# Optimization experiments

Measured on AMD Instinct MI355X. Metric: run time of the kernel, lower is better.

Reference implementation:

```python
import jax, jax.numpy as jnp
import numpy as np

HIDDEN = 2048
INTER = 1024
N_EXPERTS = 8
TOP_K = 2
B, S = 1, 2048


def setup_inputs() -> dict:
    key = jax.random.key(0)
    k1, k2, k3, k4, k5, k6 = jax.random.split(key, 6)
    x = jax.random.normal(k1, (B, S, HIDDEN), dtype=jnp.float32)
    expert_indices = jax.random.randint(k2, (B, S, TOP_K), 0, N_EXPERTS, dtype=jnp.int64)
    expert_weights = jax.random.uniform(k3, (B, S, TOP_K), dtype=jnp.float32)
    gate_proj = jax.random.normal(k4, (N_EXPERTS, INTER, HIDDEN), dtype=jnp.float32) * 0.02
    up_proj = jax.random.normal(k5, (N_EXPERTS, INTER, HIDDEN), dtype=jnp.float32) * 0.02
    down_proj = jax.random.normal(k6, (N_EXPERTS, HIDDEN, INTER), dtype=jnp.float32) * 0.02
    return {"x": x, "expert_indices": expert_indices, "expert_weights": expert_weights,
            "gate_proj": gate_proj, "up_proj": up_proj, "down_proj": down_proj}


def reference(x, expert_indices, expert_weights, gate_proj, up_proj, down_proj):
    b, s, h = x.shape
    e = gate_proj.shape[0]
    xf = x.reshape(-1, h)                                   # [T, H]
    idx = expert_indices.reshape(-1, expert_indices.shape[-1])   # [T, K]
    wts = expert_weights.reshape(-1, expert_weights.shape[-1])   # [T, K]
    # Combine weights per (token, expert); duplicate expert slots sum, matching index_add_.
    comb = jnp.sum(jax.nn.one_hot(idx, e, dtype=xf.dtype) * wts[..., None], axis=1)  # [T, E]
    # SwiGLU expert MLP, computed densely over all experts then masked by routing weights.
    g = jnp.einsum('th,eih->tei', xf, gate_proj)            # [T, E, I]
    u = jnp.einsum('th,eih->tei', xf, up_proj)              # [T, E, I]
    inter = jax.nn.silu(g) * u                              # [T, E, I]
    out = jnp.einsum('tei,ehi->th', inter * comb[:, :, None], down_proj)  # [T, H]
    return out.reshape(b, s, h)
```

## Files before the change

### kernel.cpp

```cpp
#include <hip/hip_runtime.h>
#include <math.h>

#define HID 2048
#define ITR 1024
#define NEXP 8
#define TOPK 2
#define NTOK 2048
#define NSLOT (NTOK * TOPK)
#define MAXTT 40
#define SLOTS 80

typedef __attribute__((ext_vector_type(8))) short short8;
typedef __attribute__((ext_vector_type(4))) float f32x4;

__device__ __forceinline__ unsigned short f2bf(float f) {
    unsigned u = __float_as_uint(f);
    u += 0x7FFFu + ((u >> 16) & 1u);
    return (unsigned short)(u >> 16);
}

#define GLL16(g, l) \
    __builtin_amdgcn_global_load_lds((const __attribute__((address_space(1))) unsigned int*)(g), \
                                     (__attribute__((address_space(3))) unsigned int*)(l), 16, 0, 0)

__global__ void route_all_k(const int* __restrict__ idx,
                            const float* __restrict__ wts,
                            int* __restrict__ counts_g,
                            int* __restrict__ btok,
                            float* __restrict__ bw,
                            int* __restrict__ offs_g,
                            int* __restrict__ slotmap,
                            int* __restrict__ gu_tab,
                            int* __restrict__ dn_tab) {
    __shared__ int h[NEXP], nt[NEXP], pre[NEXP], base[NEXP], cur[NEXP];
    const int tid = threadIdx.x;
    if (tid < NEXP) { h[tid] = 0; cur[tid] = 0; }
    __syncthreads();
    for (int s = tid; s < NSLOT; s += 256) atomicAdd(&h[idx[s]], 1);
    __syncthreads();
    if (tid == 0) {
        int a = 0;
        for (int e = 0; e < NEXP; ++e) {
            base[e] = a; counts_g[e] = h[e]; offs_g[e] = a;
            int t = (h[e] + 127) >> 7; nt[e] = t; a += t << 7;
        }
        int p = 0;
        for (int e = 0; e < NEXP; ++e) { pre[e] = p; p += nt[e]; }
    }
    __syncthreads();
    for (int s = tid; s < NSLOT; s += 256) {
        int e = idx[s];
        int p = atomicAdd(&cur[e], 1);
        btok[e * NSLOT + p] = s >> 1;
        bw[e * NSLOT + p] = wts[s];
        slotmap[s] = base[e] + p;
    }
    for (int i = tid; i < 8 * SLOTS; i += 256) { gu_tab[i] = -1; dn_tab[i] = -1; }
    __syncthreads();
    if (tid < 128) {
        int c = tid, e = c >> 4, ib = c & 15;
        int sb = 2 * pre[e] + (ib >> 3) * nt[e];
        for (int j = 0; j < nt[e]; ++j)
            gu_tab[(sb + j) * 8 + (ib & 7)] = (e << 16) | (ib << 8) | j;
    } else {
        int c = tid - 128, e = c >> 4, ib = c & 15;
        int sb = 2 * pre[e] + (ib >> 3) * nt[e];
        for (int j = 0; j < nt[e]; ++j)
            dn_tab[(sb + j) * 8 + (ib & 7)] = (e << 16) | (ib << 8) | j;
    }
}

__device__ __forceinline__ void cvt8(const float* __restrict__ src,
                                     unsigned short* __restrict__ dst, size_t o) {
    const float4* s4 = (const float4*)src + o * 2;
    float4 a = s4[0], b = s4[1];
    union { unsigned short s[8]; uint4 v; } r;
    r.s[0] = f2bf(a.x); r.s[1] = f2bf(a.y); r.s[2] = f2bf(a.z); r.s[3] = f2bf(a.w);
    r.s[4] = f2bf(b.x); r.s[5] = f2bf(b.y); r.s[6] = f2bf(b.z); r.s[7] = f2bf(b.w);
    ((uint4*)dst)[o] = r.v;
}

__global__ void cvt_gux_k(const float* __restrict__ x, const float* __restrict__ g,
                          const float* __restrict__ u,
                          unsigned short* __restrict__ xb, unsigned short* __restrict__ gb,
                          unsigned short* __restrict__ ub) {
    size_t j = (size_t)blockIdx.x * 256 + threadIdx.x;
    const size_t X8 = (size_t)NTOK * HID / 8;
    const size_t W8 = (size_t)NEXP * ITR * HID / 8;
    if (j < X8)           cvt8(x, xb, j);
    else if (j < X8 + W8) cvt8(g, gb, j - X8);
    else                  cvt8(u, ub, j - X8 - W8);
}

__global__ void cvt_dn_k(const float* __restrict__ d, unsigned short* __restrict__ db) {
    size_t j = (size_t)blockIdx.x * 256 + threadIdx.x;
    cvt8(d, db, j);
}

__global__ void combine_k(const float* __restrict__ part,
                          const int* __restrict__ slotmap,
                          float* __restrict__ out) {
    int gid = blockIdx.x * 256 + threadIdx.x;
    int t = gid >> 9;
    int c = gid & 511;
    int s0 = slotmap[t * 2], s1 = slotmap[t * 2 + 1];
    float4 a = ((const float4*)part)[(size_t)s0 * 512 + c];
    float4 b = ((const float4*)part)[(size_t)s1 * 512 + c];
    float4 r; r.x = a.x + b.x; r.y = a.y + b.y; r.z = a.z + b.z; r.w = a.w + b.w;
    ((float4*)out)[gid] = r;
}

#define BK 64

__launch_bounds__(256)
__global__ void moe_gu_bf_k(const unsigned short* __restrict__ xb,
                            const unsigned short* __restrict__ gateb,
                            const unsigned short* __restrict__ upb,
                            const int* __restrict__ counts,
                            const int* __restrict__ btok,
                            const int* __restrict__ off,
                            const int* __restrict__ gu_tab,
                            unsigned short* __restrict__ interw) {
    const int v = gu_tab[blockIdx.x];
    if (v < 0) return;
    const int e    = v >> 16;
    const int iblk = (v >> 8) & 255;
    const int tile = v & 255;
    const int n = counts[e];

    __shared__ unsigned short s_a[128 * 64];
    __shared__ unsigned short s_bg[64 * 64];
    __shared__ unsigned short s_bu[64 * 64];
    __shared__ int s_tok[128];

    const int tid = threadIdx.x;
    if (tid < 128) {
        int tt = tile * 128 + tid;
        s_tok[tid] = btok[e * NSLOT + (tt < n ? tt : n - 1)];
    }
    __syncthreads();

    const int w = tid >> 6;
    const int lane = tid & 63;

    const char* asrc[4]; unsigned short* adst[4];
    #pragma unroll
    for (int t = 0; t < 4; ++t) {
        int c = tid + t * 256;
        int r = c >> 3;
        unsigned sw = ((unsigned)(c & 7) * 16u) ^ (((unsigned)r & 7u) << 4);
        asrc[t] = (const char*)xb + (size_t)s_tok[r] * (HID * 2) + sw;
        adst[t] = s_a + (size_t)(t * 256 + w * 64) * 8;
    }
    const char* gB = (const char*)gateb + ((size_t)e * ITR + (size_t)iblk * 64) * (HID * 2);
    const char* uB = (const char*)upb   + ((size_t)e * ITR + (size_t)iblk * 64) * (HID * 2);
    const char* gsrc[2]; const char* usrc[2];
    unsigned short* gdst[2]; unsigned short* udst[2];
    #pragma unroll
    for (int t = 0; t < 2; ++t) {
        int c = tid + t * 256;
        int r = c >> 3;
        unsigned sw = ((unsigned)(c & 7) * 16u) ^ (((unsigned)r & 7u) << 4);
        gsrc[t] = gB + (size_t)r * (HID * 2) + sw;
        usrc[t] = uB + (size_t)r * (HID * 2) + sw;
        gdst[t] = s_bg + (size_t)(t * 256 + w * 64) * 8;
        udst[t] = s_bu + (size_t)(t * 256 + w * 64) * 8;
    }

    const int wm = (w & 1) * 64, wn = (w >> 1) * 32;
    const int l15 = lane & 15, quad = lane >> 4;

    f32x4 accg[4][2], accu[4][2];
    #pragma unroll
    for (int m = 0; m < 4; ++m)
        #pragma unroll
        for (int nn = 0; nn < 2; ++nn) {
            accg[m][nn] = (f32x4){0.f, 0.f, 0.f, 0.f};
            accu[m][nn] = (f32x4){0.f, 0.f, 0.f, 0.f};
        }

    for (int k0 = 0; k0 < HID; k0 += BK) {
        const int kb0 = k0 * 2;
        #pragma unroll
        for (int t = 0; t < 4; ++t) GLL16(asrc[t] + kb0, adst[t]);
        #pragma unroll
        for (int t = 0; t < 2; ++t) { GLL16(gsrc[t] + kb0, gdst[t]); GLL16(usrc[t] + kb0, udst[t]); }
        __syncthreads();
        #pragma unroll
        for (int kk = 0; kk < 2; ++kk) {
            const unsigned kbyte = (unsigned)(kk * 64 + quad * 16);
            short8 af[4], bg[2], bu[2];
            #pragma unroll
            for (int m = 0; m < 4; ++m) {
                unsigned r = (unsigned)(wm + m * 16 + l15);
                af[m] = *(const short8*)&s_a[r * 64 + ((kbyte ^ ((r & 7u) << 4)) >> 1)];
            }
            #pragma unroll
            for (int nn = 0; nn < 2; ++nn) {
                unsigned r = (unsigned)(wn + nn * 16 + l15);
                unsigned co = (kbyte ^ ((r & 7u) << 4)) >> 1;
                bg[nn] = *(const short8*)&s_bg[r * 64 + co];
                bu[nn] = *(const short8*)&s_bu[r * 64 + co];
            }
            #pragma unroll
            for (int m = 0; m < 4; ++m)
                #pragma unroll
                for (int nn = 0; nn < 2; ++nn) {
                    accg[m][nn] = __builtin_amdgcn_mfma_f32_16x16x32_bf16(af[m], bg[nn], accg[m][nn], 0, 0, 0);
                    accu[m][nn] = __builtin_amdgcn_mfma_f32_16x16x32_bf16(af[m], bu[nn], accu[m][nn], 0, 0, 0);
                }
        }
        __syncthreads();
    }

    const int pos0 = off[e] + tile * 128;
    #pragma unroll
    for (int m = 0; m < 4; ++m) {
        #pragma unroll
        for (int nn = 0; nn < 2; ++nn) {
            int col = iblk * 64 + wn + nn * 16 + l15;
            #pragma unroll
            for (int r = 0; r < 4; ++r) {
                int row = wm + m * 16 + quad * 4 + r;
                float g = accg[m][nn][r], u = accu[m][nn][r];
                float s = g / (1.0f + __expf(-g));
                interw[(size_t)(pos0 + row) * ITR + col] = f2bf(s * u);
            }
        }
    }
}

__launch_bounds__(256)
__global__ void moe_down_bf_k(const unsigned short* __restrict__ interw,
                              const unsigned short* __restrict__ downb,
                              const int* __restrict__ counts,
                              const int* __restrict__ btok,
                              const float* __restrict__ bw,
                              const int* __restrict__ off,
                              const int* __restrict__ dn_tab,
                              float* __restrict__ dst,
                              int mode) {
    const int v = dn_tab[blockIdx.x];
    if (v < 0) return;
    const int e    = v >> 16;
    const int hblk = (v >> 8) & 255;
    const int tile = v & 255;
    const int n = counts[e];

    __shared__ unsigned short s_a[128 * 64];
    __shared__ unsigned short s_b[128 * 64];
    __shared__ int s_tok[128];
    __shared__ float s_w[128];

    const int tid = threadIdx.x;
    if (tid < 128) {
        int tt = tile * 128 + tid;
        bool vv = tt < n;
        s_tok[tid] = btok[e * NSLOT + (vv ? tt : n - 1)];
        s_w[tid] = vv ? bw[e * NSLOT + tt] : 0.0f;
    }
    __syncthreads();

    const int w = tid >> 6;
    const int lane = tid & 63;
    const int pos0 = off[e] + tile * 128;

    const char* asrc[4]; unsigned short* adst[4];
    const char* bsrc[4]; unsigned short* bdst[4];
    const char* dB = (const char*)downb + ((size_t)e * HID + (size_t)hblk * 128) * (ITR * 2);
    #pragma unroll
    for (int t = 0; t < 4; ++t) {
        int c = tid + t * 256;
        int r = c >> 3;
        unsigned sw = ((unsigned)(c & 7) * 16u) ^ (((unsigned)r & 7u) << 4);
        asrc[t] = (const char*)interw + (size_t)(pos0 + r) * (ITR * 2) + sw;
        bsrc[t] = dB + (size_t)r * (ITR * 2) + sw;
        adst[t] = s_a + (size_t)(t * 256 + w * 64) * 8;
        bdst[t] = s_b + (size_t)(t * 256 + w * 64) * 8;
    }

    const int wm = (w & 1) * 64, wn = (w >> 1) * 64;
    const int l15 = lane & 15, quad = lane >> 4;

    f32x4 acc[4][4];
    #pragma unroll
    for (int m = 0; m < 4; ++m)
        #pragma unroll
        for (int nn = 0; nn < 4; ++nn) acc[m][nn] = (f32x4){0.f, 0.f, 0.f, 0.f};

    for (int k0 = 0; k0 < ITR; k0 += BK) {
        const int kb0 = k0 * 2;
        #pragma unroll
        for (int t = 0; t < 4; ++t) GLL16(asrc[t] + kb0, adst[t]);
        #pragma unroll
        for (int t = 0; t < 4; ++t) GLL16(bsrc[t] + kb0, bdst[t]);
        __syncthreads();
        #pragma unroll
        for (int kk = 0; kk < 2; ++kk) {
            const unsigned kbyte = (unsigned)(kk * 64 + quad * 16);
            short8 af[4], bf[4];
            #pragma unroll
            for (int m = 0; m < 4; ++m) {
                unsigned r = (unsigned)(wm + m * 16 + l15);
                af[m] = *(const short8*)&s_a[r * 64 + ((kbyte ^ ((r & 7u) << 4)) >> 1)];
            }
            #pragma unroll
            for (int nn = 0; nn < 4; ++nn) {
                unsigned r = (unsigned)(wn + nn * 16 + l15);
                bf[nn] = *(const short8*)&s_b[r * 64 + ((kbyte ^ ((r & 7u) << 4)) >> 1)];
            }
            #pragma unroll
            for (int m = 0; m < 4; ++m)
                #pragma unroll
                for (int nn = 0; nn < 4; ++nn)
                    acc[m][nn] = __builtin_amdgcn_mfma_f32_16x16x32_bf16(af[m], bf[nn], acc[m][nn], 0, 0, 0);
        }
        __syncthreads();
    }

    if (mode == 0) {
        #pragma unroll
        for (int m = 0; m < 4; ++m) {
            #pragma unroll
            for (int nn = 0; nn < 4; ++nn) {
                int col = hblk * 128 + wn + nn * 16 + l15;
                #pragma unroll
                for (int r = 0; r < 4; ++r) {
                    int row = wm + m * 16 + quad * 4 + r;
                    dst[(size_t)(pos0 + row) * HID + col] = s_w[row] * acc[m][nn][r];
                }
            }
        }
    } else {
        #pragma unroll
        for (int m = 0; m < 4; ++m) {
            #pragma unroll
            for (int nn = 0; nn < 4; ++nn) {
                int col = hblk * 128 + wn + nn * 16 + l15;
                #pragma unroll
                for (int r = 0; r < 4; ++r) {
                    int row = wm + m * 16 + quad * 4 + r;
                    atomicAdd(&dst[(size_t)s_tok[row] * HID + col], s_w[row] * acc[m][nn][r]);
                }
            }
        }
    }
}

#define LDW 72

__global__ void xconv_k(const float* __restrict__ x, unsigned short* __restrict__ xb) {
    int i = blockIdx.x * blockDim.x + threadIdx.x;
    float4 v = ((const float4*)x)[i];
    ushort4 b;
    b.x = f2bf(v.x); b.y = f2bf(v.y); b.z = f2bf(v.z); b.w = f2bf(v.w);
    ((ushort4*)xb)[i] = b;
}

__launch_bounds__(256)
__global__ void moe_gu_k(const unsigned short* __restrict__ xb,
                         const float* __restrict__ gate,
                         const float* __restrict__ up,
                         const int* __restrict__ counts,
                         const int* __restrict__ btok,
                         const int* __restrict__ off,
                         const int* __restrict__ gu_tab,
                         unsigned short* __restrict__ interw) {
    const int v = gu_tab[blockIdx.x];
    if (v < 0) return;
    const int e    = v >> 16;
    const int iblk = (v >> 8) & 255;
    const int tile = v & 255;
    const int n = counts[e];

    __shared__ unsigned short s_a[128][LDW];
    __shared__ unsigned short s_bg[64][LDW];
    __shared__ unsigned short s_bu[64][LDW];
    __shared__ int s_tok[128];

    const int tid = threadIdx.x;
    if (tid < 128) {
        int tt = tile * 128 + tid;
        s_tok[tid] = btok[e * NSLOT + (tt < n ? tt : n - 1)];
    }
    __syncthreads();

    const unsigned short* asrc[4];
    unsigned aoff[4];
    #pragma unroll
    for (int t = 0; t < 4; ++t) {
        int c = tid + t * 256;
        int r = c >> 3, col = (c & 7) * 8;
        asrc[t] = xb + (size_t)s_tok[r] * HID + col;
        aoff[t] = r * LDW + col;
    }
    const float* gbase = gate + (size_t)e * ITR * HID + (size_t)iblk * 64 * HID;
    const float* ubase = up   + (size_t)e * ITR * HID + (size_t)iblk * 64 * HID;
    unsigned boff[4], loff[4];
    #pragma unroll
    for (int t = 0; t < 4; ++t) {
        int f = tid + t * 256;
        int r = f >> 4, col = (f & 15) * 4;
        boff[t] = r * HID + col;
        loff[t] = r * LDW + col;
    }

    const int lane = tid & 63;
    const int w = tid >> 6;
    const int wm = (w & 1) * 64, wn = (w >> 1) * 32;
    const int l15 = lane & 15, quad = lane >> 4;

    f32x4 accg[4][2], accu[4][2];
    #pragma unroll
    for (int m = 0; m < 4; ++m)
        #pragma unroll
        for (int nn = 0; nn < 2; ++nn) {
            accg[m][nn] = (f32x4){0.f, 0.f, 0.f, 0.f};
            accu[m][nn] = (f32x4){0.f, 0.f, 0.f, 0.f};
        }

    unsigned short* s_flat_a = &s_a[0][0];
    unsigned short* s_flat_g = &s_bg[0][0];
    unsigned short* s_flat_u = &s_bu[0][0];

    uint4 pa[4];
    float4 pg[4], pu[4];
    #pragma unroll
    for (int t = 0; t < 4; ++t) {
        pa[t] = *(const uint4*)(asrc[t]);
        pg[t] = *(const float4*)(gbase + boff[t]);
        pu[t] = *(const float4*)(ubase + boff[t]);
    }

    for (int k0 = 0; k0 < HID; k0 += BK) {
        #pragma unroll
        for (int t = 0; t < 4; ++t) {
            *(uint4*)(s_flat_a + aoff[t]) = pa[t];
            ushort4 gb, ub;
            gb.x = f2bf(pg[t].x); gb.y = f2bf(pg[t].y); gb.z = f2bf(pg[t].z); gb.w = f2bf(pg[t].w);
            ub.x = f2bf(pu[t].x); ub.y = f2bf(pu[t].y); ub.z = f2bf(pu[t].z); ub.w = f2bf(pu[t].w);
            *(ushort4*)(s_flat_g + loff[t]) = gb;
            *(ushort4*)(s_flat_u + loff[t]) = ub;
        }
        __syncthreads();
        if (k0 + BK < HID) {
            #pragma unroll
            for (int t = 0; t < 4; ++t) {
                pa[t] = *(const uint4*)(asrc[t] + k0 + BK);
                pg[t] = *(const float4*)(gbase + boff[t] + k0 + BK);
                pu[t] = *(const float4*)(ubase + boff[t] + k0 + BK);
            }
        }
        #pragma unroll
        for (int kk = 0; kk < 2; ++kk) {
            const int kc = kk * 32 + quad * 8;
            short8 af[4], bg[2], bu[2];
            #pragma unroll
            for (int m = 0; m < 4; ++m)
                af[m] = *(const short8*)&s_a[wm + m * 16 + l15][kc];
            #pragma unroll
            for (int nn = 0; nn < 2; ++nn) {
                bg[nn] = *(const short8*)&s_bg[wn + nn * 16 + l15][kc];
                bu[nn] = *(const short8*)&s_bu[wn + nn * 16 + l15][kc];
            }
            #pragma unroll
            for (int m = 0; m < 4; ++m)
                #pragma unroll
                for (int nn = 0; nn < 2; ++nn) {
                    accg[m][nn] = __builtin_amdgcn_mfma_f32_16x16x32_bf16(af[m], bg[nn], accg[m][nn], 0, 0, 0);
                    accu[m][nn] = __builtin_amdgcn_mfma_f32_16x16x32_bf16(af[m], bu[nn], accu[m][nn], 0, 0, 0);
                }
        }
        __syncthreads();
    }

    const int pos0 = off[e] + tile * 128;
    #pragma unroll
    for (int m = 0; m < 4; ++m) {
        #pragma unroll
        for (int nn = 0; nn < 2; ++nn) {
            int col = iblk * 64 + wn + nn * 16 + l15;
            #pragma unroll
            for (int r = 0; r < 4; ++r) {
                int row = wm + m * 16 + quad * 4 + r;
                float g = accg[m][nn][r], u = accu[m][nn][r];
                float s = g / (1.0f + __expf(-g));
                interw[(size_t)(pos0 + row) * ITR + col] = f2bf(s * u);
            }
        }
    }
}

__launch_bounds__(256)
__global__ void moe_down_k(const unsigned short* __restrict__ interw,
                           const float* __restrict__ down,
                           const int* __restrict__ counts,
                           const int* __restrict__ btok,
                           const float* __restrict__ bw,
                           const int* __restrict__ off,
                           const int* __restrict__ dn_tab,
                           float* __restrict__ dst,
                           int mode) {
    const int v = dn_tab[blockIdx.x];
    if (v < 0) return;
    const int e    = v >> 16;
    const int hblk = (v >> 8) & 255;
    const int tile = v & 255;
    const int n = counts[e];

    __shared__ unsigned short s_a[128][LDW];
    __shared__ unsigned short s_b[128][LDW];
    __shared__ int s_tok[128];
    __shared__ float s_w[128];

    const int tid = threadIdx.x;
    if (tid < 128) {
        int tt = tile * 128 + tid;
        bool vv = tt < n;
        s_tok[tid] = btok[e * NSLOT + (vv ? tt : n - 1)];
        s_w[tid] = vv ? bw[e * NSLOT + tt] : 0.0f;
    }
    __syncthreads();

    const int pos0 = off[e] + tile * 128;
    unsigned aoff[4], asrco[4];
    #pragma unroll
    for (int t = 0; t < 4; ++t) {
        int c = tid + t * 256;
        int r = c >> 3, col = (c & 7) * 8;
        asrco[t] = (unsigned)((pos0 + r) * ITR + col);
        aoff[t] = r * LDW + col;
    }
    const float* dbase = down + (size_t)e * HID * ITR + (size_t)hblk * 128 * ITR;
    unsigned boff[8], loff[8];
    #pragma unroll
    for (int t = 0; t < 8; ++t) {
        int f = tid + t * 256;
        int r = f >> 4, col = (f & 15) * 4;
        boff[t] = r * ITR + col;
        loff[t] = r * LDW + col;
    }

    const int lane = tid & 63;
    const int w = tid >> 6;
    const int wm = (w & 1) * 64, wn = (w >> 1) * 64;
    const int l15 = lane & 15, quad = lane >> 4;

    f32x4 acc[4][4];
    #pragma unroll
    for (int m = 0; m < 4; ++m)
        #pragma unroll
        for (int nn = 0; nn < 4; ++nn) acc[m][nn] = (f32x4){0.f, 0.f, 0.f, 0.f};

    unsigned short* s_flat_a = &s_a[0][0];
    unsigned short* s_flat_b = &s_b[0][0];

    uint4 pa[4];
    float4 pb[8];
    #pragma unroll
    for (int t = 0; t < 4; ++t) pa[t] = *(const uint4*)(interw + asrco[t]);
    #pragma unroll
    for (int t = 0; t < 8; ++t) pb[t] = *(const float4*)(dbase + boff[t]);

    for (int k0 = 0; k0 < ITR; k0 += BK) {
        #pragma unroll
        for (int t = 0; t < 4; ++t)
            *(uint4*)(s_flat_a + aoff[t]) = pa[t];
        #pragma unroll
        for (int t = 0; t < 8; ++t) {
            ushort4 b;
            b.x = f2bf(pb[t].x); b.y = f2bf(pb[t].y); b.z = f2bf(pb[t].z); b.w = f2bf(pb[t].w);
            *(ushort4*)(s_flat_b + loff[t]) = b;
        }
        __syncthreads();
        if (k0 + BK < ITR) {
            #pragma unroll
            for (int t = 0; t < 4; ++t) pa[t] = *(const uint4*)(interw + asrco[t] + k0 + BK);
            #pragma unroll
            for (int t = 0; t < 8; ++t) pb[t] = *(const float4*)(dbase + boff[t] + k0 + BK);
        }
        #pragma unroll
        for (int kk = 0; kk < 2; ++kk) {
            const int kc = kk * 32 + quad * 8;
            short8 af[4], bf[4];
            #pragma unroll
            for (int m = 0; m < 4; ++m)
                af[m] = *(const short8*)&s_a[wm + m * 16 + l15][kc];
            #pragma unroll
            for (int nn = 0; nn < 4; ++nn)
                bf[nn] = *(const short8*)&s_b[wn + nn * 16 + l15][kc];
            #pragma unroll
            for (int m = 0; m < 4; ++m)
                #pragma unroll
                for (int nn = 0; nn < 4; ++nn)
                    acc[m][nn] = __builtin_amdgcn_mfma_f32_16x16x32_bf16(af[m], bf[nn], acc[m][nn], 0, 0, 0);
        }
        __syncthreads();
    }

    if (mode == 0) {
        #pragma unroll
        for (int m = 0; m < 4; ++m) {
            #pragma unroll
            for (int nn = 0; nn < 4; ++nn) {
                int col = hblk * 128 + wn + nn * 16 + l15;
                #pragma unroll
                for (int r = 0; r < 4; ++r) {
                    int row = wm + m * 16 + quad * 4 + r;
                    dst[(size_t)(pos0 + row) * HID + col] = s_w[row] * acc[m][nn][r];
                }
            }
        }
    } else {
        #pragma unroll
        for (int m = 0; m < 4; ++m) {
            #pragma unroll
            for (int nn = 0; nn < 4; ++nn) {
                int col = hblk * 128 + wn + nn * 16 + l15;
                #pragma unroll
                for (int r = 0; r < 4; ++r) {
                    int row = wm + m * 16 + quad * 4 + r;
                    atomicAdd(&dst[(size_t)s_tok[row] * HID + col], s_w[row] * acc[m][nn][r]);
                }
            }
        }
    }
}

#define TT 8
#define TN 128
#define TK 16
#define WPAD 20
#define IPAD 1028
#define MAXTILES (NSLOT / TT)

__global__ void route_k(const int* __restrict__ idx,
                        const float* __restrict__ wts,
                        int* __restrict__ counts,
                        int* __restrict__ btok,
                        float* __restrict__ bw) {
    int s = blockIdx.x * blockDim.x + threadIdx.x;
    if (s >= NSLOT) return;
    int e = idx[s];
    int pos = atomicAdd(&counts[e], 1);
    btok[(size_t)e * NSLOT + pos] = s / TOPK;
    bw[(size_t)e * NSLOT + pos] = wts[s];
}

__launch_bounds__(256)
__global__ void moe_k(const float* __restrict__ x,
                      const float* __restrict__ gate,
                      const float* __restrict__ up,
                      const float* __restrict__ down,
                      const int* __restrict__ counts,
                      const int* __restrict__ btok,
                      const float* __restrict__ bw,
                      float* __restrict__ out) {
    const int e = blockIdx.x / MAXTILES;
    const int tile = blockIdx.x % MAXTILES;
    const int n = counts[e];
    const int t0 = tile * TT;
    if (t0 >= n) return;

    __shared__ float s_wg[TN][WPAD];
    __shared__ float s_wu[TN][WPAD];
    __shared__ float s_it[TT][IPAD];
    __shared__ int   s_tok[TT];
    __shared__ float s_w[TT];

    const int tid = threadIdx.x;
    if (tid < TT) {
        int tt = t0 + tid;
        bool v = tt < n;
        s_tok[tid] = btok[(size_t)e * NSLOT + (v ? tt : t0)];
        s_w[tid] = v ? bw[(size_t)e * NSLOT + tt] : 0.0f;
    }
    __syncthreads();

    const int tok = tid >> 5;
    const int ic  = (tid & 31) << 2;
    const int mytok = s_tok[tok];
    const float* xrow = x + (size_t)mytok * HID;
    const float* gbase = gate + (size_t)e * ITR * HID;
    const float* ubase = up   + (size_t)e * ITR * HID;
    const float* dbase = down + (size_t)e * HID * ITR;

    for (int i0 = 0; i0 < ITR; i0 += TN) {
        float ag[4] = {0.f, 0.f, 0.f, 0.f};
        float au[4] = {0.f, 0.f, 0.f, 0.f};
        for (int k0 = 0; k0 < HID; k0 += TK) {
            #pragma unroll
            for (int j = 0; j < 2; ++j) {
                int f4 = tid + j * 256;
                int r = f4 >> 2, c = (f4 & 3) << 2;
                *(float4*)&s_wg[r][c] = *(const float4*)(gbase + (size_t)(i0 + r) * HID + k0 + c);
                *(float4*)&s_wu[r][c] = *(const float4*)(ubase + (size_t)(i0 + r) * HID + k0 + c);
            }
            __syncthreads();
            #pragma unroll
            for (int kk = 0; kk < TK; kk += 4) {
                float4 xv = *(const float4*)(xrow + k0 + kk);
                #pragma unroll
                for (int q = 0; q < 4; ++q) {
                    float4 wg = *(const float4*)&s_wg[ic + q][kk];
                    float4 wu = *(const float4*)&s_wu[ic + q][kk];
                    ag[q] += xv.x * wg.x + xv.y * wg.y + xv.z * wg.z + xv.w * wg.w;
                    au[q] += xv.x * wu.x + xv.y * wu.y + xv.z * wu.z + xv.w * wu.w;
                }
            }
            __syncthreads();
        }
        #pragma unroll
        for (int q = 0; q < 4; ++q) {
            float g = ag[q], u = au[q];
            s_it[tok][i0 + ic + q] = (g / (1.0f + __expf(-g))) * u;
        }
    }
    __syncthreads();

    const float wscale = s_w[tok];
    for (int h0 = 0; h0 < HID; h0 += TN) {
        float ac[4] = {0.f, 0.f, 0.f, 0.f};
        for (int k0 = 0; k0 < ITR; k0 += TK) {
            #pragma unroll
            for (int j = 0; j < 2; ++j) {
                int f4 = tid + j * 256;
                int r = f4 >> 2, c = (f4 & 3) << 2;
                *(float4*)&s_wg[r][c] = *(const float4*)(dbase + (size_t)(h0 + r) * ITR + k0 + c);
            }
            __syncthreads();
            #pragma unroll
            for (int kk = 0; kk < TK; kk += 4) {
                float4 xv = *(const float4*)&s_it[tok][k0 + kk];
                #pragma unroll
                for (int q = 0; q < 4; ++q) {
                    float4 wv = *(const float4*)&s_wg[ic + q][kk];
                    ac[q] += xv.x * wv.x + xv.y * wv.y + xv.z * wv.z + xv.w * wv.w;
                }
            }
            __syncthreads();
        }
        float* orow = out + (size_t)mytok * HID + h0 + ic;
        #pragma unroll
        for (int q = 0; q < 4; ++q) atomicAdd(&orow[q], wscale * ac[q]);
    }
}

extern "C" void kernel_launch(void* const* d_in, const int* in_sizes, int n_in,
                              void* d_out, int out_size, void* d_ws, size_t ws_size,
                              hipStream_t stream) {
    const float* x    = (const float*)d_in[0];
    const int*   idx  = (const int*)d_in[1];
    const float* wts  = (const float*)d_in[2];
    const float* gate = (const float*)d_in[3];
    const float* up   = (const float*)d_in[4];
    const float* down = (const float*)d_in[5];
    float* out = (float*)d_out;

    const size_t off_btok  = 256;
    const size_t off_bw    = off_btok + (size_t)NEXP * NSLOT * 4;
    const size_t off_offs  = off_bw + (size_t)NEXP * NSLOT * 4;
    const size_t off_smap  = off_offs + 256;
    const size_t off_tabs  = off_smap + (size_t)NSLOT * 4;
    const size_t off_xb    = off_tabs + 2 * 8 * SLOTS * 4;

    const size_t off_inter_o = off_xb + (size_t)NTOK * HID * 2;
    const size_t off_part_o  = off_inter_o + (size_t)(MAXTT * 128) * ITR * 2;
    const size_t need_mid  = off_part_o;
    const size_t need_full = off_part_o + (size_t)(MAXTT * 128) * HID * 4;

    const size_t XBSZ  = (size_t)NTOK * HID * 2;
    const size_t WSZ   = (size_t)NEXP * ITR * HID * 2;
    const size_t INTSZ = (size_t)(MAXTT * 128) * ITR * 2;
    const size_t off_gb      = off_xb + XBSZ;
    const size_t off_ub      = off_gb + WSZ;
    const size_t off_inter_n = off_ub + WSZ;
    const size_t off_db      = off_xb;
    const size_t off_part_n  = off_db + WSZ;
    const size_t need_bf     = off_inter_n + INTSZ;

    int*   counts = (int*)d_ws;
    int*   btok   = (int*)((char*)d_ws + off_btok);
    float* bwp    = (float*)((char*)d_ws + off_bw);
    int*   offs   = (int*)((char*)d_ws + off_offs);
    int*   smap   = (int*)((char*)d_ws + off_smap);
    int*   gu_tab = (int*)((char*)d_ws + off_tabs);
    int*   dn_tab = gu_tab + 8 * SLOTS;
    unsigned short* xb = (unsigned short*)((char*)d_ws + off_xb);

    if (ws_size >= need_bf) {
        unsigned short* gb     = (unsigned short*)((char*)d_ws + off_gb);
        unsigned short* ub     = (unsigned short*)((char*)d_ws + off_ub);
        unsigned short* db     = (unsigned short*)((char*)d_ws + off_db);
        unsigned short* interw = (unsigned short*)((char*)d_ws + off_inter_n);
        float*          part   = (float*)((char*)d_ws + off_part_n);

        const int cvt1_blocks = (int)(((size_t)NTOK * HID / 8 + 2 * (WSZ / 16)) / 256);
        const int cvt2_blocks = (int)((WSZ / 16) / 256);

        route_all_k<<<dim3(1), dim3(256), 0, stream>>>(idx, wts, counts, btok, bwp, offs, smap, gu_tab, dn_tab);
        cvt_gux_k<<<dim3(cvt1_blocks), dim3(256), 0, stream>>>(x, gate, up, xb, gb, ub);
        moe_gu_bf_k<<<dim3(8 * SLOTS), dim3(256), 0, stream>>>(xb, gb, ub, counts, btok, offs, gu_tab, interw);
        cvt_dn_k<<<dim3(cvt2_blocks), dim3(256), 0, stream>>>(down, db);
        moe_down_bf_k<<<dim3(8 * SLOTS), dim3(256), 0, stream>>>(interw, db, counts, btok, bwp, offs, dn_tab, part, 0);
        combine_k<<<dim3(NTOK * HID / 4 / 256), dim3(256), 0, stream>>>(part, smap, out);
    } else if (ws_size >= need_mid) {
        const int full = (ws_size >= need_full);
        unsigned short* interw = (unsigned short*)((char*)d_ws + off_inter_o);
        float* part   = (float*)((char*)d_ws + off_part_o);
        route_all_k<<<dim3(1), dim3(256), 0, stream>>>(idx, wts, counts, btok, bwp, offs, smap, gu_tab, dn_tab);
        xconv_k<<<dim3(NTOK * HID / 4 / 256), dim3(256), 0, stream>>>(x, xb);
        if (!full) hipMemsetAsync(d_out, 0, (size_t)out_size * sizeof(float), stream);
        moe_gu_k<<<dim3(8 * SLOTS), dim3(256), 0, stream>>>(xb, gate, up, counts, btok, offs, gu_tab, interw);
        moe_down_k<<<dim3(8 * SLOTS), dim3(256), 0, stream>>>(interw, down, counts, btok, bwp, offs, dn_tab,
                                                              full ? part : out, full ? 0 : 1);
        if (full)
            combine_k<<<dim3(NTOK * HID / 4 / 256), dim3(256), 0, stream>>>(part, smap, out);
    } else {
        hipMemsetAsync(d_out, 0, (size_t)out_size * sizeof(float), stream);
        hipMemsetAsync(counts, 0, 256, stream);
        route_k<<<dim3((NSLOT + 255) / 256), dim3(256), 0, stream>>>(idx, wts, counts, btok, bwp);
        moe_k<<<dim3(NEXP * MAXTILES), dim3(256), 0, stream>>>(x, gate, up, down, counts, btok, bwp, out);
    }
}
```

Before: 360.5 us.

## Double-buffer LDS tiles in expert GEMMs and fuse routing with all weight conversion

Both expert GEMM kernels now use two LDS buffers. The next K-slice is loaded with global_load_lds while the current slice feeds the MFMAs, which replaces the per-iteration load-then-sync pattern. When workspace allows, a new prep kernel folds routing and the bf16 conversion of x, gate, up and down into one launch, using a workspace layout that keeps all converted weights resident at once. This cuts kernel launches and overlaps memory latency with compute. The cost is doubled LDS use, which may lower occupancy, and a larger workspace requirement.

```diff
diff --git a/kernel.cpp b/kernel.cpp
--- a/kernel.cpp
+++ b/kernel.cpp
@@ -23,15 +23,15 @@
     __builtin_amdgcn_global_load_lds((const __attribute__((address_space(1))) unsigned int*)(g), \
                                      (__attribute__((address_space(3))) unsigned int*)(l), 16, 0, 0)
 
-__global__ void route_all_k(const int* __restrict__ idx,
-                            const float* __restrict__ wts,
-                            int* __restrict__ counts_g,
-                            int* __restrict__ btok,
-                            float* __restrict__ bw,
-                            int* __restrict__ offs_g,
-                            int* __restrict__ slotmap,
-                            int* __restrict__ gu_tab,
-                            int* __restrict__ dn_tab) {
+__device__ __forceinline__ void route_body(const int* __restrict__ idx,
+                                           const float* __restrict__ wts,
+                                           int* __restrict__ counts_g,
+                                           int* __restrict__ btok,
+                                           float* __restrict__ bw,
+                                           int* __restrict__ offs_g,
+                                           int* __restrict__ slotmap,
+                                           int* __restrict__ gu_tab,
+                                           int* __restrict__ dn_tab) {
     __shared__ int h[NEXP], nt[NEXP], pre[NEXP], base[NEXP], cur[NEXP];
     const int tid = threadIdx.x;
     if (tid < NEXP) { h[tid] = 0; cur[tid] = 0; }
@@ -62,12 +62,20 @@
         int sb = 2 * pre[e] + (ib >> 3) * nt[e];
         for (int j = 0; j < nt[e]; ++j)
             gu_tab[(sb + j) * 8 + (ib & 7)] = (e << 16) | (ib << 8) | j;
-    } else {
+    } else if (tid < 256) {
         int c = tid - 128, e = c >> 4, ib = c & 15;
         int sb = 2 * pre[e] + (ib >> 3) * nt[e];
         for (int j = 0; j < nt[e]; ++j)
             dn_tab[(sb + j) * 8 + (ib & 7)] = (e << 16) | (ib << 8) | j;
     }
+}
+
+__global__ void route_all_k(const int* __restrict__ idx, const float* __restrict__ wts,
+                            int* __restrict__ counts_g, int* __restrict__ btok,
+                            float* __restrict__ bw, int* __restrict__ offs_g,
+                            int* __restrict__ slotmap, int* __restrict__ gu_tab,
+                            int* __restrict__ dn_tab) {
+    route_body(idx, wts, counts_g, btok, bw, offs_g, slotmap, gu_tab, dn_tab);
 }
 
 __device__ __forceinline__ void cvt8(const float* __restrict__ src,
@@ -78,6 +86,28 @@
     r.s[0] = f2bf(a.x); r.s[1] = f2bf(a.y); r.s[2] = f2bf(a.z); r.s[3] = f2bf(a.w);
     r.s[4] = f2bf(b.x); r.s[5] = f2bf(b.y); r.s[6] = f2bf(b.z); r.s[7] = f2bf(b.w);
     ((uint4*)dst)[o] = r.v;
+}
+
+__global__ void prep_all_k(const float* __restrict__ x, const float* __restrict__ g,
+                           const float* __restrict__ u, const float* __restrict__ d,
+                           const int* __restrict__ idx, const float* __restrict__ wts,
+                           unsigned short* __restrict__ xb, unsigned short* __restrict__ gb,
+                           unsigned short* __restrict__ ub, unsigned short* __restrict__ db,
+                           int* __restrict__ counts_g, int* __restrict__ btok,
+                           float* __restrict__ bw, int* __restrict__ offs_g,
+                           int* __restrict__ slotmap, int* __restrict__ gu_tab,
+                           int* __restrict__ dn_tab) {
+    if (blockIdx.x == 0) {
+        route_body(idx, wts, counts_g, btok, bw, offs_g, slotmap, gu_tab, dn_tab);
+        return;
+    }
+    size_t j = (size_t)(blockIdx.x - 1) * 256 + threadIdx.x;
+    const size_t X8 = (size_t)NTOK * HID / 8;
+    const size_t W8 = (size_t)NEXP * ITR * HID / 8;
+    if (j < X8)                cvt8(x, xb, j);
+    else if (j < X8 + W8)      cvt8(g, gb, j - X8);
+    else if (j < X8 + 2 * W8)  cvt8(u, ub, j - X8 - W8);
+    else                       cvt8(d, db, j - X8 - 2 * W8);
 }
 
 __global__ void cvt_gux_k(const float* __restrict__ x, const float* __restrict__ g,
@@ -128,9 +158,9 @@
     const int tile = v & 255;
     const int n = counts[e];
 
-    __shared__ unsigned short s_a[128 * 64];
-    __shared__ unsigned short s_bg[64 * 64];
-    __shared__ unsigned short s_bu[64 * 64];
+    __shared__ unsigned short s_a[2 * 128 * 64];
+    __shared__ unsigned short s_bg[2 * 64 * 64];
+    __shared__ unsigned short s_bu[2 * 64 * 64];
     __shared__ int s_tok[128];
 
     const int tid = threadIdx.x;
@@ -143,19 +173,18 @@
     const int w = tid >> 6;
     const int lane = tid & 63;
 
-    const char* asrc[4]; unsigned short* adst[4];
+    const char* asrc[4]; unsigned aoff[4];
     #pragma unroll
     for (int t = 0; t < 4; ++t) {
         int c = tid + t * 256;
         int r = c >> 3;
         unsigned sw = ((unsigned)(c & 7) * 16u) ^ (((unsigned)r & 7u) << 4);
         asrc[t] = (const char*)xb + (size_t)s_tok[r] * (HID * 2) + sw;
-        adst[t] = s_a + (size_t)(t * 256 + w * 64) * 8;
+        aoff[t] = (unsigned)(t * 256 + w * 64) * 8;
     }
     const char* gB = (const char*)gateb + ((size_t)e * ITR + (size_t)iblk * 64) * (HID * 2);
     const char* uB = (const char*)upb   + ((size_t)e * ITR + (size_t)iblk * 64) * (HID * 2);
-    const char* gsrc[2]; const char* usrc[2];
-    unsigned short* gdst[2]; unsigned short* udst[2];
+    const char* gsrc[2]; const char* usrc[2]; unsigned boff[2];
     #pragma unroll
     for (int t = 0; t < 2; ++t) {
         int c = tid + t * 256;
@@ -163,8 +192,7 @@
         unsigned sw = ((unsigned)(c & 7) * 16u) ^ (((unsigned)r & 7u) << 4);
         gsrc[t] = gB + (size_t)r * (HID * 2) + sw;
         usrc[t] = uB + (size_t)r * (HID * 2) + sw;
-        gdst[t] = s_bg + (size_t)(t * 256 + w * 64) * 8;
-        udst[t] = s_bu + (size_t)(t * 256 + w * 64) * 8;
+        boff[t] = (unsigned)(t * 256 + w * 64) * 8;
     }
 
     const int wm = (w & 1) * 64, wn = (w >> 1) * 32;
@@ -179,13 +207,30 @@
             accu[m][nn] = (f32x4){0.f, 0.f, 0.f, 0.f};
         }
 
+    #pragma unroll
+    for (int t = 0; t < 4; ++t) GLL16(asrc[t], s_a + aoff[t]);
+    #pragma unroll
+    for (int t = 0; t < 2; ++t) { GLL16(gsrc[t], s_bg + boff[t]); GLL16(usrc[t], s_bu + boff[t]); }
+    asm volatile("s_waitcnt vmcnt(0)" ::: "memory");
+    __builtin_amdgcn_s_barrier();
+
+    int cur = 0;
     for (int k0 = 0; k0 < HID; k0 += BK) {
-        const int kb0 = k0 * 2;
-        #pragma unroll
-        for (int t = 0; t < 4; ++t) GLL16(asrc[t] + kb0, adst[t]);
-        #pragma unroll
-        for (int t = 0; t < 2; ++t) { GLL16(gsrc[t] + kb0, gdst[t]); GLL16(usrc[t] + kb0, udst[t]); }
-        __syncthreads();
+        if (k0 + BK < HID) {
+            const int kb = (k0 + BK) * 2;
+            const unsigned bo_a = (unsigned)(cur ^ 1) * 8192;
+            const unsigned bo_b = (unsigned)(cur ^ 1) * 4096;
+            #pragma unroll
+            for (int t = 0; t < 4; ++t) GLL16(asrc[t] + kb, s_a + bo_a + aoff[t]);
+            #pragma unroll
+            for (int t = 0; t < 2; ++t) {
+                GLL16(gsrc[t] + kb, s_bg + bo_b + boff[t]);
+                GLL16(usrc[t] + kb, s_bu + bo_b + boff[t]);
+            }
+        }
+        const unsigned short* pa = s_a + (unsigned)cur * 8192;
+        const unsigned short* pg = s_bg + (unsigned)cur * 4096;
+        const unsigned short* pu = s_bu + (unsigned)cur * 4096;
         #pragma unroll
         for (int kk = 0; kk < 2; ++kk) {
             const unsigned kbyte = (unsigned)(kk * 64 + quad * 16);
@@ -193,14 +238,14 @@
             #pragma unroll
             for (int m = 0; m < 4; ++m) {
                 unsigned r = (unsigned)(wm + m * 16 + l15);
-                af[m] = *(const short8*)&s_a[r * 64 + ((kbyte ^ ((r & 7u) << 4)) >> 1)];
+                af[m] = *(const short8*)&pa[r * 64 + ((kbyte ^ ((r & 7u) << 4)) >> 1)];
             }
             #pragma unroll
             for (int nn = 0; nn < 2; ++nn) {
                 unsigned r = (unsigned)(wn + nn * 16 + l15);
                 unsigned co = (kbyte ^ ((r & 7u) << 4)) >> 1;
-                bg[nn] = *(const short8*)&s_bg[r * 64 + co];
-                bu[nn] = *(const short8*)&s_bu[r * 64 + co];
+                bg[nn] = *(const short8*)&pg[r * 64 + co];
+                bu[nn] = *(const short8*)&pu[r * 64 + co];
             }
             #pragma unroll
             for (int m = 0; m < 4; ++m)
@@ -210,7 +255,9 @@
                     accu[m][nn] = __builtin_amdgcn_mfma_f32_16x16x32_bf16(af[m], bu[nn], accu[m][nn], 0, 0, 0);
                 }
         }
-        __syncthreads();
+        asm volatile("s_waitcnt vmcnt(0)" ::: "memory");
+        __builtin_amdgcn_s_barrier();
+        cur ^= 1;
     }
 
     const int pos0 = off[e] + tile * 128;
@@ -247,8 +294,8 @@
     const int tile = v & 255;
     const int n = counts[e];
 
-    __shared__ unsigned short s_a[128 * 64];
-    __shared__ unsigned short s_b[128 * 64];
+    __shared__ unsigned short s_a[2 * 128 * 64];
+    __shared__ unsigned short s_b[2 * 128 * 64];
     __shared__ int s_tok[128];
     __shared__ float s_w[128];
 
@@ -265,8 +312,7 @@
     const int lane = tid & 63;
     const int pos0 = off[e] + tile * 128;
 
-    const char* asrc[4]; unsigned short* adst[4];
-    const char* bsrc[4]; unsigned short* bdst[4];
+    const char* asrc[4]; const char* bsrc[4]; unsigned loff[4];
     const char* dB = (const char*)downb + ((size_t)e * HID + (size_t)hblk * 128) * (ITR * 2);
     #pragma unroll
     for (int t = 0; t < 4; ++t) {
@@ -275,8 +321,7 @@
         unsigned sw = ((unsigned)(c & 7) * 16u) ^ (((unsigned)r & 7u) << 4);
         asrc[t] = (const char*)interw + (size_t)(pos0 + r) * (ITR * 2) + sw;
         bsrc[t] = dB + (size_t)r * (ITR * 2) + sw;
-        adst[t] = s_a + (size_t)(t * 256 + w * 64) * 8;
-        bdst[t] = s_b + (size_t)(t * 256 + w * 64) * 8;
+        loff[t] = (unsigned)(t * 256 + w * 64) * 8;
     }
 
     const int wm = (w & 1) * 64, wn = (w >> 1) * 64;
@@ -288,13 +333,25 @@
         #pragma unroll
         for (int nn = 0; nn < 4; ++nn) acc[m][nn] = (f32x4){0.f, 0.f, 0.f, 0.f};
 
+    #pragma unroll
+    for (int t = 0; t < 4; ++t) GLL16(asrc[t], s_a + loff[t]);
+    #pragma unroll
+    for (int t = 0; t < 4; ++t) GLL16(bsrc[t], s_b + loff[t]);
+    asm volatile("s_waitcnt vmcnt(0)" ::: "memory");
+    __builtin_amdgcn_s_barrier();
+
+    int cur = 0;
     for (int k0 = 0; k0 < ITR; k0 += BK) {
-        const int kb0 = k0 * 2;
-        #pragma unroll
-        for (int t = 0; t < 4; ++t) GLL16(asrc[t] + kb0, adst[t]);
-        #pragma unroll
-        for (int t = 0; t < 4; ++t) GLL16(bsrc[t] + kb0, bdst[t]);
-        __syncthreads();
+        if (k0 + BK < ITR) {
+            const int kb = (k0 + BK) * 2;
+            const unsigned bo = (unsigned)(cur ^ 1) * 8192;
+            #pragma unroll
+            for (int t = 0; t < 4; ++t) GLL16(asrc[t] + kb, s_a + bo + loff[t]);
+            #pragma unroll
+            for (int t = 0; t < 4; ++t) GLL16(bsrc[t] + kb, s_b + bo + loff[t]);
+        }
+        const unsigned short* pa = s_a + (unsigned)cur * 8192;
+        const unsigned short* pb = s_b + (unsigned)cur * 8192;
         #pragma unroll
         for (int kk = 0; kk < 2; ++kk) {
             const unsigned kbyte = (unsigned)(kk * 64 + quad * 16);
@@ -302,12 +359,12 @@
             #pragma unroll
             for (int m = 0; m < 4; ++m) {
                 unsigned r = (unsigned)(wm + m * 16 + l15);
-                af[m] = *(const short8*)&s_a[r * 64 + ((kbyte ^ ((r & 7u) << 4)) >> 1)];
+                af[m] = *(const short8*)&pa[r * 64 + ((kbyte ^ ((r & 7u) << 4)) >> 1)];
             }
             #pragma unroll
             for (int nn = 0; nn < 4; ++nn) {
                 unsigned r = (unsigned)(wn + nn * 16 + l15);
-                bf[nn] = *(const short8*)&s_b[r * 64 + ((kbyte ^ ((r & 7u) << 4)) >> 1)];
+                bf[nn] = *(const short8*)&pb[r * 64 + ((kbyte ^ ((r & 7u) << 4)) >> 1)];
             }
             #pragma unroll
             for (int m = 0; m < 4; ++m)
@@ -315,7 +372,9 @@
                 for (int nn = 0; nn < 4; ++nn)
                     acc[m][nn] = __builtin_amdgcn_mfma_f32_16x16x32_bf16(af[m], bf[nn], acc[m][nn], 0, 0, 0);
         }
-        __syncthreads();
+        asm volatile("s_waitcnt vmcnt(0)" ::: "memory");
+        __builtin_amdgcn_s_barrier();
+        cur ^= 1;
     }
 
     if (mode == 0) {
@@ -764,20 +823,29 @@
     const size_t off_tabs  = off_smap + (size_t)NSLOT * 4;
     const size_t off_xb    = off_tabs + 2 * 8 * SLOTS * 4;
 
-    const size_t off_inter_o = off_xb + (size_t)NTOK * HID * 2;
-    const size_t off_part_o  = off_inter_o + (size_t)(MAXTT * 128) * ITR * 2;
-    const size_t need_mid  = off_part_o;
-    const size_t need_full = off_part_o + (size_t)(MAXTT * 128) * HID * 4;
-
     const size_t XBSZ  = (size_t)NTOK * HID * 2;
     const size_t WSZ   = (size_t)NEXP * ITR * HID * 2;
     const size_t INTSZ = (size_t)(MAXTT * 128) * ITR * 2;
-    const size_t off_gb      = off_xb + XBSZ;
-    const size_t off_ub      = off_gb + WSZ;
-    const size_t off_inter_n = off_ub + WSZ;
-    const size_t off_db      = off_xb;
-    const size_t off_part_n  = off_db + WSZ;
-    const size_t need_bf     = off_inter_n + INTSZ;
+    const size_t PARTSZ = (size_t)(MAXTT * 128) * HID * 4;
+
+    const size_t off_inter_o = off_xb + XBSZ;
+    const size_t off_part_o  = off_inter_o + INTSZ;
+    const size_t need_mid  = off_part_o;
+    const size_t need_full = off_part_o + PARTSZ;
+
+    const size_t off_gb2      = off_xb + XBSZ;
+    const size_t off_ub2      = off_gb2 + WSZ;
+    const size_t off_inter_n  = off_ub2 + WSZ;
+    const size_t off_db2      = off_xb;
+    const size_t off_part2    = off_db2 + WSZ;
+    const size_t need_bf      = off_inter_n + INTSZ;
+
+    const size_t off_gb1    = off_xb + XBSZ;
+    const size_t off_ub1    = off_gb1 + WSZ;
+    const size_t off_db1    = off_ub1 + WSZ;
+    const size_t off_int1   = off_db1 + WSZ;
+    const size_t off_part1  = off_gb1;
+    const size_t need_bf1   = off_int1 + INTSZ;
 
     int*   counts = (int*)d_ws;
     int*   btok   = (int*)((char*)d_ws + off_btok);
@@ -788,12 +856,29 @@
     int*   dn_tab = gu_tab + 8 * SLOTS;
     unsigned short* xb = (unsigned short*)((char*)d_ws + off_xb);
 
-    if (ws_size >= need_bf) {
-        unsigned short* gb     = (unsigned short*)((char*)d_ws + off_gb);
-        unsigned short* ub     = (unsigned short*)((char*)d_ws + off_ub);
-        unsigned short* db     = (unsigned short*)((char*)d_ws + off_db);
+    if (ws_size >= need_bf1) {
+        unsigned short* gb     = (unsigned short*)((char*)d_ws + off_gb1);
+        unsigned short* ub     = (unsigned short*)((char*)d_ws + off_ub1);
+        unsigned short* db     = (unsigned short*)((char*)d_ws + off_db1);
+        unsigned short* interw = (unsigned short*)((char*)d_ws + off_int1);
+        float*          part   = (float*)((char*)d_ws + off_part1);
+
+        const size_t X8 = (size_t)NTOK * HID / 8;
+        const size_t W8 = (size_t)NEXP * ITR * HID / 8;
+        const int prep_blocks = (int)((X8 + 3 * W8) / 256) + 1;
+
+        prep_all_k<<<dim3(prep_blocks), dim3(256), 0, stream>>>(x, gate, up, down, idx, wts,
+                                                                xb, gb, ub, db,
+                                                                counts, btok, bwp, offs, smap, gu_tab, dn_tab);
+        moe_gu_bf_k<<<dim3(8 * SLOTS), dim3(256), 0, stream>>>(xb, gb, ub, counts, btok, offs, gu_tab, interw);
+        moe_down_bf_k<<<dim3(8 * SLOTS), dim3(256), 0, stream>>>(interw, db, counts, btok, bwp, offs, dn_tab, part, 0);
+        combine_k<<<dim3(NTOK * HID / 4 / 256), dim3(256), 0, stream>>>(part, smap, out);
+    } else if (ws_size >= need_bf) {
+        unsigned short* gb     = (unsigned short*)((char*)d_ws + off_gb2);
+        unsigned short* ub     = (unsigned short*)((char*)d_ws + off_ub2);
+        unsigned short* db     = (unsigned short*)((char*)d_ws + off_db2);
         unsigned short* interw = (unsigned short*)((char*)d_ws + off_inter_n);
-        float*          part   = (float*)((char*)d_ws + off_part_n);
+        float*          part   = (float*)((char*)d_ws + off_part2);
 
         const int cvt1_blocks = (int)(((size_t)NTOK * HID / 8 + 2 * (WSZ / 16)) / 256);
         const int cvt2_blocks = (int)((WSZ / 16) / 256);
```

After: 353.5 us. Within noise of the previous version (-2.0%).

## Fuse routing into conversion prep and overlap down-proj cast with gate/up GEMM

Applied to the files above, without the earlier changes.

Merges the single-block routing kernel into a grid-stride bf16 conversion kernel, so block 0 does routing while the others convert x, gate and up. The down-projection fp32-to-bf16 conversion moves into extra blocks of the gate/up GEMM launch so it overlaps the GEMM instead of running as a separate kernel. This cuts the launch count and the serialization gaps between kernels. In exchange the workspace grows by one extra bf16 weight buffer, and the conversion blocks compete with GEMM tiles for compute units and memory bandwidth.

```diff
diff --git a/kernel.cpp b/kernel.cpp
--- a/kernel.cpp
+++ b/kernel.cpp
@@ -9,6 +9,8 @@
 #define NSLOT (NTOK * TOPK)
 #define MAXTT 40
 #define SLOTS 80
+#define CVTD_BLOCKS 2048
+#define PREP_BLOCKS 4096
 
 typedef __attribute__((ext_vector_type(8))) short short8;
 typedef __attribute__((ext_vector_type(4))) float f32x4;
@@ -23,15 +25,15 @@
     __builtin_amdgcn_global_load_lds((const __attribute__((address_space(1))) unsigned int*)(g), \
                                      (__attribute__((address_space(3))) unsigned int*)(l), 16, 0, 0)
 
-__global__ void route_all_k(const int* __restrict__ idx,
-                            const float* __restrict__ wts,
-                            int* __restrict__ counts_g,
-                            int* __restrict__ btok,
-                            float* __restrict__ bw,
-                            int* __restrict__ offs_g,
-                            int* __restrict__ slotmap,
-                            int* __restrict__ gu_tab,
-                            int* __restrict__ dn_tab) {
+__device__ __forceinline__ void route_body(const int* __restrict__ idx,
+                                           const float* __restrict__ wts,
+                                           int* __restrict__ counts_g,
+                                           int* __restrict__ btok,
+                                           float* __restrict__ bw,
+                                           int* __restrict__ offs_g,
+                                           int* __restrict__ slotmap,
+                                           int* __restrict__ gu_tab,
+                                           int* __restrict__ dn_tab) {
     __shared__ int h[NEXP], nt[NEXP], pre[NEXP], base[NEXP], cur[NEXP];
     const int tid = threadIdx.x;
     if (tid < NEXP) { h[tid] = 0; cur[tid] = 0; }
@@ -62,12 +64,20 @@
         int sb = 2 * pre[e] + (ib >> 3) * nt[e];
         for (int j = 0; j < nt[e]; ++j)
             gu_tab[(sb + j) * 8 + (ib & 7)] = (e << 16) | (ib << 8) | j;
-    } else {
+    } else if (tid < 256) {
         int c = tid - 128, e = c >> 4, ib = c & 15;
         int sb = 2 * pre[e] + (ib >> 3) * nt[e];
         for (int j = 0; j < nt[e]; ++j)
             dn_tab[(sb + j) * 8 + (ib & 7)] = (e << 16) | (ib << 8) | j;
     }
+}
+
+__global__ void route_all_k(const int* __restrict__ idx, const float* __restrict__ wts,
+                            int* __restrict__ counts_g, int* __restrict__ btok,
+                            float* __restrict__ bw, int* __restrict__ offs_g,
+                            int* __restrict__ slotmap, int* __restrict__ gu_tab,
+                            int* __restrict__ dn_tab) {
+    route_body(idx, wts, counts_g, btok, bw, offs_g, slotmap, gu_tab, dn_tab);
 }
 
 __device__ __forceinline__ void cvt8(const float* __restrict__ src,
@@ -78,6 +88,40 @@
     r.s[0] = f2bf(a.x); r.s[1] = f2bf(a.y); r.s[2] = f2bf(a.z); r.s[3] = f2bf(a.w);
     r.s[4] = f2bf(b.x); r.s[5] = f2bf(b.y); r.s[6] = f2bf(b.z); r.s[7] = f2bf(b.w);
     ((uint4*)dst)[o] = r.v;
+}
+
+__global__ void prep_all_k(const float* __restrict__ x, const float* __restrict__ g,
+                           const float* __restrict__ u,
+                           const int* __restrict__ idx, const float* __restrict__ wts,
+                           unsigned short* __restrict__ xb, unsigned short* __restrict__ gb,
+                           unsigned short* __restrict__ ub,
+                           int* __restrict__ counts_g, int* __restrict__ btok,
+                           float* __restrict__ bw, int* __restrict__ offs_g,
+                           int* __restrict__ slotmap, int* __restrict__ gu_tab,
+                           int* __restrict__ dn_tab) {
+    if (blockIdx.x == 0) {
+        route_body(idx, wts, counts_g, btok, bw, offs_g, slotmap, gu_tab, dn_tab);
+        return;
+    }
+    const size_t X8 = (size_t)NTOK * HID / 8;
+    const size_t W8 = (size_t)NEXP * ITR * HID / 8;
+    const size_t TOT = X8 + 2 * W8;
+    const size_t stride = (size_t)PREP_BLOCKS * 256;
+    size_t j = (size_t)(blockIdx.x - 1) * 256 + threadIdx.x;
+    for (; j + stride < TOT; j += 2 * stride) {
+        size_t j2 = j + stride;
+        if (j < X8)                cvt8(x, xb, j);
+        else if (j < X8 + W8)      cvt8(g, gb, j - X8);
+        else                       cvt8(u, ub, j - X8 - W8);
+        if (j2 < X8)               cvt8(x, xb, j2);
+        else if (j2 < X8 + W8)     cvt8(g, gb, j2 - X8);
+        else                       cvt8(u, ub, j2 - X8 - W8);
+    }
+    if (j < TOT) {
+        if (j < X8)                cvt8(x, xb, j);
+        else if (j < X8 + W8)      cvt8(g, gb, j - X8);
+        else                       cvt8(u, ub, j - X8 - W8);
+    }
 }
 
 __global__ void cvt_gux_k(const float* __restrict__ x, const float* __restrict__ g,
@@ -113,14 +157,27 @@
 #define BK 64
 
 __launch_bounds__(256)
-__global__ void moe_gu_bf_k(const unsigned short* __restrict__ xb,
-                            const unsigned short* __restrict__ gateb,
-                            const unsigned short* __restrict__ upb,
-                            const int* __restrict__ counts,
-                            const int* __restrict__ btok,
-                            const int* __restrict__ off,
-                            const int* __restrict__ gu_tab,
-                            unsigned short* __restrict__ interw) {
+__global__ void moe_gu_fused_k(const unsigned short* __restrict__ xb,
+                               const unsigned short* __restrict__ gateb,
+                               const unsigned short* __restrict__ upb,
+                               const int* __restrict__ counts,
+                               const int* __restrict__ btok,
+                               const int* __restrict__ off,
+                               const int* __restrict__ gu_tab,
+                               unsigned short* __restrict__ interw,
+                               const float* __restrict__ down,
+                               unsigned short* __restrict__ db) {
+    if (blockIdx.x >= 8 * SLOTS) {
+        const size_t D8 = (size_t)NEXP * HID * ITR / 8;
+        const size_t stride = (size_t)CVTD_BLOCKS * 256;
+        size_t j = (size_t)(blockIdx.x - 8 * SLOTS) * 256 + threadIdx.x;
+        for (; j + stride < D8; j += 2 * stride) {
+            cvt8(down, db, j);
+            cvt8(down, db, j + stride);
+        }
+        if (j < D8) cvt8(down, db, j);
+        return;
+    }
     const int v = gu_tab[blockIdx.x];
     if (v < 0) return;
     const int e    = v >> 16;
@@ -764,20 +821,29 @@
     const size_t off_tabs  = off_smap + (size_t)NSLOT * 4;
     const size_t off_xb    = off_tabs + 2 * 8 * SLOTS * 4;
 
-    const size_t off_inter_o = off_xb + (size_t)NTOK * HID * 2;
-    const size_t off_part_o  = off_inter_o + (size_t)(MAXTT * 128) * ITR * 2;
-    const size_t need_mid  = off_part_o;
-    const size_t need_full = off_part_o + (size_t)(MAXTT * 128) * HID * 4;
-
     const size_t XBSZ  = (size_t)NTOK * HID * 2;
     const size_t WSZ   = (size_t)NEXP * ITR * HID * 2;
     const size_t INTSZ = (size_t)(MAXTT * 128) * ITR * 2;
-    const size_t off_gb      = off_xb + XBSZ;
-    const size_t off_ub      = off_gb + WSZ;
-    const size_t off_inter_n = off_ub + WSZ;
-    const size_t off_db      = off_xb;
-    const size_t off_part_n  = off_db + WSZ;
-    const size_t need_bf     = off_inter_n + INTSZ;
+    const size_t PARTSZ = (size_t)(MAXTT * 128) * HID * 4;
+
+    const size_t off_inter_o = off_xb + XBSZ;
+    const size_t off_part_o  = off_inter_o + INTSZ;
+    const size_t need_mid  = off_part_o;
+    const size_t need_full = off_part_o + PARTSZ;
+
+    const size_t off_gb2      = off_xb + XBSZ;
+    const size_t off_ub2      = off_gb2 + WSZ;
+    const size_t off_inter_n  = off_ub2 + WSZ;
+    const size_t off_db2      = off_xb;
+    const size_t off_part2    = off_db2 + WSZ;
+    const size_t need_bf      = off_inter_n + INTSZ;
+
+    const size_t off_gb1    = off_xb + XBSZ;
+    const size_t off_ub1    = off_gb1 + WSZ;
+    const size_t off_db1    = off_ub1 + WSZ;
+    const size_t off_int1   = off_db1 + WSZ;
+    const size_t off_part1  = off_gb1;
+    const size_t need_bf1   = off_int1 + INTSZ;
 
     int*   counts = (int*)d_ws;
     int*   btok   = (int*)((char*)d_ws + off_btok);
@@ -788,19 +854,34 @@
     int*   dn_tab = gu_tab + 8 * SLOTS;
     unsigned short* xb = (unsigned short*)((char*)d_ws + off_xb);
 
-    if (ws_size >= need_bf) {
-        unsigned short* gb     = (unsigned short*)((char*)d_ws + off_gb);
-        unsigned short* ub     = (unsigned short*)((char*)d_ws + off_ub);
-        unsigned short* db     = (unsigned short*)((char*)d_ws + off_db);
+    if (ws_size >= need_bf1) {
+        unsigned short* gb     = (unsigned short*)((char*)d_ws + off_gb1);
+        unsigned short* ub     = (unsigned short*)((char*)d_ws + off_ub1);
+        unsigned short* db     = (unsigned short*)((char*)d_ws + off_db1);
+        unsigned short* interw = (unsigned short*)((char*)d_ws + off_int1);
+        float*          part   = (float*)((char*)d_ws + off_part1);
+
+        prep_all_k<<<dim3(PREP_BLOCKS + 1), dim3(256), 0, stream>>>(x, gate, up, idx, wts,
+                                                                    xb, gb, ub,
+                                                                    counts, btok, bwp, offs, smap, gu_tab, dn_tab);
+        moe_gu_fused_k<<<dim3(8 * SLOTS + CVTD_BLOCKS), dim3(256), 0, stream>>>(xb, gb, ub, counts, btok, offs,
+                                                                                gu_tab, interw, down, db);
+        moe_down_bf_k<<<dim3(8 * SLOTS), dim3(256), 0, stream>>>(interw, db, counts, btok, bwp, offs, dn_tab, part, 0);
+        combine_k<<<dim3(NTOK * HID / 4 / 256), dim3(256), 0, stream>>>(part, smap, out);
+    } else if (ws_size >= need_bf) {
+        unsigned short* gb     = (unsigned short*)((char*)d_ws + off_gb2);
+        unsigned short* ub     = (unsigned short*)((char*)d_ws + off_ub2);
+        unsigned short* db     = (unsigned short*)((char*)d_ws + off_db2);
         unsigned short* interw = (unsigned short*)((char*)d_ws + off_inter_n);
-        float*          part   = (float*)((char*)d_ws + off_part_n);
+        float*          part   = (float*)((char*)d_ws + off_part2);
 
         const int cvt1_blocks = (int)(((size_t)NTOK * HID / 8 + 2 * (WSZ / 16)) / 256);
         const int cvt2_blocks = (int)((WSZ / 16) / 256);
 
         route_all_k<<<dim3(1), dim3(256), 0, stream>>>(idx, wts, counts, btok, bwp, offs, smap, gu_tab, dn_tab);
         cvt_gux_k<<<dim3(cvt1_blocks), dim3(256), 0, stream>>>(x, gate, up, xb, gb, ub);
-        moe_gu_bf_k<<<dim3(8 * SLOTS), dim3(256), 0, stream>>>(xb, gb, ub, counts, btok, offs, gu_tab, interw);
+        moe_gu_fused_k<<<dim3(8 * SLOTS), dim3(256), 0, stream>>>(xb, gb, ub, counts, btok, offs,
+                                                                  gu_tab, interw, (const float*)0, (unsigned short*)0);
         cvt_dn_k<<<dim3(cvt2_blocks), dim3(256), 0, stream>>>(down, db);
         moe_down_bf_k<<<dim3(8 * SLOTS), dim3(256), 0, stream>>>(interw, db, counts, btok, bwp, offs, dn_tab, part, 0);
         combine_k<<<dim3(NTOK * HID / 4 / 256), dim3(256), 0, stream>>>(part, smap, out);
```

Result: faster. 345.1 us (-4.3%).
